# Optimization experiments

Hardware: AMD Instinct MI355X
Metric: run time of the kernel (lower is better)

## Reference

```python
import jax, jax.numpy as jnp
import numpy as np

N_NODES = 50000
N_EDGES = 800000
D_IN = 128
D_HID = 128
D_OUT = 1
N_GRAPHS = 64


def gcn_conv(x, edge_index, W, b):
    """PyG GCNConv: add self-loops, symmetric deg^-1/2 normalization, xW, scatter-add, +bias."""
    n = x.shape[0]
    loops = jnp.arange(n, dtype=edge_index.dtype)
    row = jnp.concatenate([edge_index[0], loops])  # source nodes
    col = jnp.concatenate([edge_index[1], loops])  # destination nodes
    deg = jax.ops.segment_sum(jnp.ones_like(col, dtype=x.dtype), col, num_segments=n)
    dinv = jax.lax.rsqrt(jnp.maximum(deg, 1.0))  # deg >= 1 due to self-loops
    norm = dinv[row] * dinv[col]                 # [E+N]
    h = x @ W                                    # [N, d_out] dense GEMM first (cheaper than per-edge)
    msgs = h[row] * norm[:, None]                # gather + scale, [E+N, d_out]
    out = jax.ops.segment_sum(msgs, col, num_segments=n)  # scatter-add
    return out + b


def setup_inputs() -> dict:
    key = jax.random.key(0)
    ks = jax.random.split(key, 12)
    x = jax.random.normal(ks[0], (N_NODES, D_IN), dtype=jnp.float32)
    edge_index = jax.random.randint(ks[1], (2, N_EDGES), 0, N_NODES, dtype=jnp.int64)
    batch = jnp.sort(jax.random.randint(ks[2], (N_NODES,), 0, N_GRAPHS, dtype=jnp.int64))
    s_in = 1.0 / np.sqrt(D_IN)
    s_hid = 1.0 / np.sqrt(D_HID)
    W0 = jax.random.uniform(ks[3], (D_IN, D_HID), jnp.float32, -s_in, s_in)
    b0 = jnp.zeros((D_HID,), jnp.float32)
    W1 = jax.random.uniform(ks[4], (D_HID, D_HID), jnp.float32, -s_hid, s_hid)
    b1 = jnp.zeros((D_HID,), jnp.float32)
    W2 = jax.random.uniform(ks[5], (D_HID, D_HID), jnp.float32, -s_hid, s_hid)
    b2 = jnp.zeros((D_HID,), jnp.float32)
    fc_w = jax.random.uniform(ks[6], (D_HID, D_OUT), jnp.float32, -s_hid, s_hid)
    fc_b = jax.random.uniform(ks[7], (D_OUT,), jnp.float32, -s_hid, s_hid)
    return {"x": x, "edge_index": edge_index, "batch": batch,
            "W0": W0, "b0": b0, "W1": W1, "b1": b1, "W2": W2, "b2": b2,
            "fc_w": fc_w, "fc_b": fc_b}


def reference(x, edge_index, batch, W0, b0, W1, b1, W2, b2, fc_w, fc_b):
    h = x
    for W, b in ((W0, b0), (W1, b1), (W2, b2)):  # 3 GCN layers (structural, not data loop)
        h = jax.nn.relu(gcn_conv(h, edge_index, W, b))
    # global_mean_pool over graph ids
    sums = jax.ops.segment_sum(h, batch, num_segments=N_GRAPHS)          # [G, d]
    counts = jax.ops.segment_sum(jnp.ones((h.shape[0],), h.dtype), batch, num_segments=N_GRAPHS)
    pooled = sums / jnp.maximum(counts, 1.0)[:, None]
    return pooled @ fc_w + fc_b  # [G, 1]
```

## Files before the change

### kernel.cpp

```cpp
#include <hip/hip_runtime.h>

#define DH 128
#define NGRAPH 64
#define NSHARD 8

static __device__ __forceinline__ float4 f4fma(float a, float4 b, float4 c) {
  c.x = fmaf(a, b.x, c.x); c.y = fmaf(a, b.y, c.y);
  c.z = fmaf(a, b.z, c.z); c.w = fmaf(a, b.w, c.w);
  return c;
}

__global__ void count_k(const int* __restrict__ col, int* __restrict__ deg8,
                        const int* __restrict__ batch, int* __restrict__ gcnt,
                        int e, int n) {
  int i = blockIdx.x * blockDim.x + threadIdx.x;
  if (i < e) {
    atomicAdd(&deg8[(blockIdx.x & (NSHARD - 1)) * n + col[i]], 1);
  }
  bool active = (i < n);
  int g = active ? batch[i] : 0;
  unsigned long long act = __ballot(active);
  if (!active) return;
  int first = __ffsll((long long)act) - 1;
  int g0 = __shfl(g, first);
  bool uni = __all(g == g0);
  int lane = threadIdx.x & 63;
  if (uni) {
    if (lane == first) atomicAdd(&gcnt[g], (int)__popcll(act));
  } else {
    atomicAdd(&gcnt[g], 1);
  }
}

__global__ __launch_bounds__(512) void scan1_k(const int* __restrict__ deg8, int* __restrict__ deg_tot,
                                               int* __restrict__ incl, int* __restrict__ blksum, int n) {
  __shared__ int s[512];
  int t = threadIdx.x;
  int i = blockIdx.x * 512 + t;
  int v = 0;
  if (i < n) {
    #pragma unroll
    for (int c = 0; c < NSHARD; ++c) v += deg8[c * n + i];
    deg_tot[i] = v;
  }
  s[t] = v;
  __syncthreads();
  #pragma unroll
  for (int off = 1; off < 512; off <<= 1) {
    int x = (t >= off) ? s[t - off] : 0;
    __syncthreads();
    s[t] += x;
    __syncthreads();
  }
  if (i < n) incl[i] = s[t];
  if (t == 511) blksum[blockIdx.x] = s[511];
}

__global__ __launch_bounds__(128) void scan2_k(int* __restrict__ blksum, int nb) {
  __shared__ int s[128];
  int t = threadIdx.x;
  int v = (t < nb) ? blksum[t] : 0;
  s[t] = v;
  __syncthreads();
  #pragma unroll
  for (int off = 1; off < 128; off <<= 1) {
    int x = (t >= off) ? s[t - off] : 0;
    __syncthreads();
    s[t] += x;
    __syncthreads();
  }
  if (t < nb) blksum[t] = s[t] - v;
}

__global__ __launch_bounds__(512) void scan3_k(const int* __restrict__ deg_tot, int* __restrict__ csr_ptr,
                                               const int* __restrict__ blkoff, int* __restrict__ cursor,
                                               float* __restrict__ dinv, int n, int e) {
  int i = blockIdx.x * 512 + threadIdx.x;
  if (i < n) {
    int cnt = deg_tot[i];
    int excl = csr_ptr[i] - cnt + blkoff[i >> 9];
    csr_ptr[i] = excl;
    cursor[i] = excl;
    dinv[i] = rsqrtf((float)(cnt + 1));
  }
  if (i == 0) csr_ptr[n] = e;
}

__global__ void scatter_k(const int* __restrict__ row, const int* __restrict__ col,
                          int* __restrict__ cursor, int* __restrict__ csr_src, int e) {
  int i = blockIdx.x * blockDim.x + threadIdx.x;
  if (i < e) {
    int c = col[i];
    int pos = atomicAdd(&cursor[c], 1);
    csr_src[pos] = row[i];
  }
}

__global__ __launch_bounds__(256) void gemm_k(const float* __restrict__ A, const float* __restrict__ W,
                                              const float* __restrict__ dinv,
                                              float* __restrict__ C, int M) {
  __shared__ float ws4[32][128];
  const int tid = threadIdx.x;
  const int tx = tid & 31;
  const int ty = tid >> 5;
  const int m_base = blockIdx.x * 64;

  const float* ar[8];
  #pragma unroll
  for (int i = 0; i < 8; i++) {
    int r = m_base + ty * 8 + i;
    if (r >= M) r = M - 1;
    ar[i] = A + (size_t)r * DH;
  }

  float4 acc[8];
  #pragma unroll
  for (int i = 0; i < 8; i++) acc[i] = make_float4(0.f, 0.f, 0.f, 0.f);

  for (int kc = 0; kc < 128; kc += 32) {
    const float4* Wg = (const float4*)(W + kc * DH);
    float4* wsv = (float4*)ws4;
    wsv[tid] = Wg[tid];
    wsv[tid + 256] = Wg[tid + 256];
    wsv[tid + 512] = Wg[tid + 512];
    wsv[tid + 768] = Wg[tid + 768];
    __syncthreads();
    #pragma unroll
    for (int k = 0; k < 32; k += 4) {
      float4 wb0 = *(const float4*)&ws4[k + 0][tx * 4];
      float4 wb1 = *(const float4*)&ws4[k + 1][tx * 4];
      float4 wb2 = *(const float4*)&ws4[k + 2][tx * 4];
      float4 wb3 = *(const float4*)&ws4[k + 3][tx * 4];
      #pragma unroll
      for (int i = 0; i < 8; i++) {
        float4 xa = *(const float4*)(ar[i] + kc + k);
        acc[i] = f4fma(xa.x, wb0, acc[i]);
        acc[i] = f4fma(xa.y, wb1, acc[i]);
        acc[i] = f4fma(xa.z, wb2, acc[i]);
        acc[i] = f4fma(xa.w, wb3, acc[i]);
      }
    }
    __syncthreads();
  }
  #pragma unroll
  for (int i = 0; i < 8; i++) {
    int r = m_base + ty * 8 + i;
    int rc = (r < M) ? r : (M - 1);
    float dsc = dinv[rc];
    acc[i].x *= dsc; acc[i].y *= dsc; acc[i].z *= dsc; acc[i].w *= dsc;
    *(float4*)(C + (size_t)r * DH + tx * 4) = acc[i];
  }
}

__global__ __launch_bounds__(256) void aggregate_k(const float* __restrict__ hs, const float* __restrict__ dinv,
                                                   const int* __restrict__ ptr, const int* __restrict__ csr_src,
                                                   const float* __restrict__ bias, float* __restrict__ out, int n) {
  int wave = threadIdx.x >> 6;
  int lane = threadIdx.x & 63;
  int node = blockIdx.x * 4 + wave;
  if (node >= n) return;
  const float2* h2 = (const float2*)hs;
  float di = dinv[node];
  int e0 = ptr[node], e1 = ptr[node + 1];
  float2 a0 = h2[(size_t)node * 64 + lane];
  float2 a1 = make_float2(0.f, 0.f), a2 = a1, a3 = a1, a4 = a1, a5 = a1, a6 = a1, a7 = a1;
  int e = e0;
  for (; e + 8 <= e1; e += 8) {
    int s0 = csr_src[e + 0], s1 = csr_src[e + 1], s2 = csr_src[e + 2], s3 = csr_src[e + 3];
    int s4 = csr_src[e + 4], s5 = csr_src[e + 5], s6 = csr_src[e + 6], s7 = csr_src[e + 7];
    float2 v0 = h2[(size_t)s0 * 64 + lane];
    float2 v1 = h2[(size_t)s1 * 64 + lane];
    float2 v2 = h2[(size_t)s2 * 64 + lane];
    float2 v3 = h2[(size_t)s3 * 64 + lane];
    float2 v4 = h2[(size_t)s4 * 64 + lane];
    float2 v5 = h2[(size_t)s5 * 64 + lane];
    float2 v6 = h2[(size_t)s6 * 64 + lane];
    float2 v7 = h2[(size_t)s7 * 64 + lane];
    a0.x += v0.x; a0.y += v0.y;
    a1.x += v1.x; a1.y += v1.y;
    a2.x += v2.x; a2.y += v2.y;
    a3.x += v3.x; a3.y += v3.y;
    a4.x += v4.x; a4.y += v4.y;
    a5.x += v5.x; a5.y += v5.y;
    a6.x += v6.x; a6.y += v6.y;
    a7.x += v7.x; a7.y += v7.y;
  }
  for (; e + 4 <= e1; e += 4) {
    int s0 = csr_src[e + 0], s1 = csr_src[e + 1], s2 = csr_src[e + 2], s3 = csr_src[e + 3];
    float2 v0 = h2[(size_t)s0 * 64 + lane];
    float2 v1 = h2[(size_t)s1 * 64 + lane];
    float2 v2 = h2[(size_t)s2 * 64 + lane];
    float2 v3 = h2[(size_t)s3 * 64 + lane];
    a0.x += v0.x; a0.y += v0.y;
    a1.x += v1.x; a1.y += v1.y;
    a2.x += v2.x; a2.y += v2.y;
    a3.x += v3.x; a3.y += v3.y;
  }
  for (; e < e1; ++e) {
    int s = csr_src[e];
    float2 v = h2[(size_t)s * 64 + lane];
    a0.x += v.x; a0.y += v.y;
  }
  float sx = ((a0.x + a1.x) + (a2.x + a3.x)) + ((a4.x + a5.x) + (a6.x + a7.x));
  float sy = ((a0.y + a1.y) + (a2.y + a3.y)) + ((a4.y + a5.y) + (a6.y + a7.y));
  float2 b = *(const float2*)(bias + lane * 2);
  sx = fmaxf(fmaf(sx, di, b.x), 0.f);
  sy = fmaxf(fmaf(sy, di, b.y), 0.f);
  ((float2*)out)[(size_t)node * 64 + lane] = make_float2(sx, sy);
}

#define POOL_CHUNK 50
__global__ __launch_bounds__(128) void pool_partial_k(const float* __restrict__ h, const int* __restrict__ batch,
                                                      float* __restrict__ pooled, int n) {
  int n0 = blockIdx.x * POOL_CHUNK;
  if (n0 >= n) return;
  int n1 = n0 + POOL_CHUNK; if (n1 > n) n1 = n;
  int d = threadIdx.x;
  float acc = 0.f;
  int gp = batch[n0];
  for (int i = n0; i < n1; ++i) {
    int g = batch[i];
    if (g != gp) { atomicAdd(&pooled[(size_t)gp * DH + d], acc); acc = 0.f; gp = g; }
    acc += h[(size_t)i * DH + d];
  }
  atomicAdd(&pooled[(size_t)gp * DH + d], acc);
}

__global__ void final_k(const float* __restrict__ pooled, const int* __restrict__ gcnt,
                        const float* __restrict__ fcw, const float* __restrict__ fcb,
                        float* __restrict__ out) {
  int g = threadIdx.x;
  if (g >= NGRAPH) return;
  float c = fmaxf((float)gcnt[g], 1.f);
  float s = 0.f;
  #pragma unroll 4
  for (int d = 0; d < DH; ++d) s = fmaf(pooled[(size_t)g * DH + d] / c, fcw[d], s);
  out[g] = s + fcb[0];
}

extern "C" void kernel_launch(void* const* d_in, const int* in_sizes, int n_in,
                              void* d_out, int out_size, void* d_ws, size_t ws_size,
                              hipStream_t stream) {
  const float* x    = (const float*)d_in[0];
  const int*   ei   = (const int*)d_in[1];
  const int*   batch= (const int*)d_in[2];
  const float* W0   = (const float*)d_in[3];
  const float* b0   = (const float*)d_in[4];
  const float* W1   = (const float*)d_in[5];
  const float* b1   = (const float*)d_in[6];
  const float* W2   = (const float*)d_in[7];
  const float* b2   = (const float*)d_in[8];
  const float* fcw  = (const float*)d_in[9];
  const float* fcb  = (const float*)d_in[10];
  float* out = (float*)d_out;

  const int N = in_sizes[0] / DH;
  const int E = in_sizes[1] / 2;
  const int* row = ei;
  const int* col = ei + E;
  const int MPAD = ((N + 63) / 64) * 64;

  char* ws = (char*)d_ws;
  size_t off = 0;
  auto carve = [&](size_t bytes) -> char* {
    char* p = ws + off;
    off = (off + bytes + 255) & ~(size_t)255;
    return p;
  };
  float* bufA    = (float*)carve((size_t)MPAD * DH * 4);
  float* bufB    = (float*)carve((size_t)MPAD * DH * 4);
  int*   deg8    = (int*)carve((size_t)NSHARD * N * 4);
  int*   deg_tot = (int*)carve((size_t)N * 4);
  float* dinv    = (float*)carve((size_t)N * 4);
  int*   csr_ptr = (int*)carve((size_t)(N + 1) * 4);
  int*   cursor  = (int*)carve((size_t)N * 4);
  int*   csr_src = (int*)carve((size_t)E * 4);
  int*   blksum  = (int*)carve(128 * 4);
  int*   gcnt    = (int*)carve(NGRAPH * 4);
  float* pooled  = (float*)carve((size_t)NGRAPH * DH * 4);
  (void)ws_size; (void)n_in; (void)out_size;

  const int nb256E = (E + 255) / 256;
  const int nbScan = (N + 511) / 512;

  hipMemsetAsync(deg8, 0, (size_t)NSHARD * N * 4, stream);
  hipMemsetAsync(gcnt, 0, NGRAPH * 4 + (size_t)NGRAPH * DH * 4, stream);

  count_k<<<nb256E, 256, 0, stream>>>(col, deg8, batch, gcnt, E, N);
  scan1_k<<<nbScan, 512, 0, stream>>>(deg8, deg_tot, csr_ptr, blksum, N);
  scan2_k<<<1, 128, 0, stream>>>(blksum, nbScan);
  scan3_k<<<nbScan, 512, 0, stream>>>(deg_tot, csr_ptr, blksum, cursor, dinv, N, E);
  scatter_k<<<nb256E, 256, 0, stream>>>(row, col, cursor, csr_src, E);

  const int gemmBlocks = MPAD / 64;
  const int aggBlocks = (N + 3) / 4;

  gemm_k<<<gemmBlocks, 256, 0, stream>>>(x, W0, dinv, bufA, N);
  aggregate_k<<<aggBlocks, 256, 0, stream>>>(bufA, dinv, csr_ptr, csr_src, b0, bufB, N);
  gemm_k<<<gemmBlocks, 256, 0, stream>>>(bufB, W1, dinv, bufA, N);
  aggregate_k<<<aggBlocks, 256, 0, stream>>>(bufA, dinv, csr_ptr, csr_src, b1, bufB, N);
  gemm_k<<<gemmBlocks, 256, 0, stream>>>(bufB, W2, dinv, bufA, N);
  aggregate_k<<<aggBlocks, 256, 0, stream>>>(bufA, dinv, csr_ptr, csr_src, b2, bufB, N);

  const int poolBlocks = (N + POOL_CHUNK - 1) / POOL_CHUNK;
  pool_partial_k<<<poolBlocks, 128, 0, stream>>>(bufB, batch, pooled, N);
  final_k<<<1, 64, 0, stream>>>(pooled, gcnt, fcw, fcb, out);
}
```

Before: 503.3 us.

## Overlap first GEMM with degree counting and shard scatter cursors

```diff
diff --git a/kernel.cpp b/kernel.cpp
--- a/kernel.cpp
+++ b/kernel.cpp
@@ -10,100 +10,15 @@
   return c;
 }
 
-__global__ void count_k(const int* __restrict__ col, int* __restrict__ deg8,
-                        const int* __restrict__ batch, int* __restrict__ gcnt,
-                        int e, int n) {
-  int i = blockIdx.x * blockDim.x + threadIdx.x;
-  if (i < e) {
-    atomicAdd(&deg8[(blockIdx.x & (NSHARD - 1)) * n + col[i]], 1);
-  }
-  bool active = (i < n);
-  int g = active ? batch[i] : 0;
-  unsigned long long act = __ballot(active);
-  if (!active) return;
-  int first = __ffsll((long long)act) - 1;
-  int g0 = __shfl(g, first);
-  bool uni = __all(g == g0);
-  int lane = threadIdx.x & 63;
-  if (uni) {
-    if (lane == first) atomicAdd(&gcnt[g], (int)__popcll(act));
-  } else {
-    atomicAdd(&gcnt[g], 1);
-  }
-}
-
-__global__ __launch_bounds__(512) void scan1_k(const int* __restrict__ deg8, int* __restrict__ deg_tot,
-                                               int* __restrict__ incl, int* __restrict__ blksum, int n) {
-  __shared__ int s[512];
-  int t = threadIdx.x;
-  int i = blockIdx.x * 512 + t;
-  int v = 0;
-  if (i < n) {
-    #pragma unroll
-    for (int c = 0; c < NSHARD; ++c) v += deg8[c * n + i];
-    deg_tot[i] = v;
-  }
-  s[t] = v;
-  __syncthreads();
-  #pragma unroll
-  for (int off = 1; off < 512; off <<= 1) {
-    int x = (t >= off) ? s[t - off] : 0;
-    __syncthreads();
-    s[t] += x;
-    __syncthreads();
-  }
-  if (i < n) incl[i] = s[t];
-  if (t == 511) blksum[blockIdx.x] = s[511];
-}
-
-__global__ __launch_bounds__(128) void scan2_k(int* __restrict__ blksum, int nb) {
-  __shared__ int s[128];
-  int t = threadIdx.x;
-  int v = (t < nb) ? blksum[t] : 0;
-  s[t] = v;
-  __syncthreads();
-  #pragma unroll
-  for (int off = 1; off < 128; off <<= 1) {
-    int x = (t >= off) ? s[t - off] : 0;
-    __syncthreads();
-    s[t] += x;
-    __syncthreads();
-  }
-  if (t < nb) blksum[t] = s[t] - v;
-}
-
-__global__ __launch_bounds__(512) void scan3_k(const int* __restrict__ deg_tot, int* __restrict__ csr_ptr,
-                                               const int* __restrict__ blkoff, int* __restrict__ cursor,
-                                               float* __restrict__ dinv, int n, int e) {
-  int i = blockIdx.x * 512 + threadIdx.x;
-  if (i < n) {
-    int cnt = deg_tot[i];
-    int excl = csr_ptr[i] - cnt + blkoff[i >> 9];
-    csr_ptr[i] = excl;
-    cursor[i] = excl;
-    dinv[i] = rsqrtf((float)(cnt + 1));
-  }
-  if (i == 0) csr_ptr[n] = e;
-}
-
-__global__ void scatter_k(const int* __restrict__ row, const int* __restrict__ col,
-                          int* __restrict__ cursor, int* __restrict__ csr_src, int e) {
-  int i = blockIdx.x * blockDim.x + threadIdx.x;
-  if (i < e) {
-    int c = col[i];
-    int pos = atomicAdd(&cursor[c], 1);
-    csr_src[pos] = row[i];
-  }
-}
-
-__global__ __launch_bounds__(256) void gemm_k(const float* __restrict__ A, const float* __restrict__ W,
-                                              const float* __restrict__ dinv,
-                                              float* __restrict__ C, int M) {
+template<bool SCALE>
+static __device__ __forceinline__ void gemm_body(const float* __restrict__ A, const float* __restrict__ W,
+                                                 const float* __restrict__ dinv, float* __restrict__ C,
+                                                 int M, int blk) {
   __shared__ float ws4[32][128];
   const int tid = threadIdx.x;
   const int tx = tid & 31;
   const int ty = tid >> 5;
-  const int m_base = blockIdx.x * 64;
+  const int m_base = blk * 64;
 
   const float* ar[8];
   #pragma unroll
@@ -145,11 +60,133 @@
   #pragma unroll
   for (int i = 0; i < 8; i++) {
     int r = m_base + ty * 8 + i;
-    int rc = (r < M) ? r : (M - 1);
-    float dsc = dinv[rc];
-    acc[i].x *= dsc; acc[i].y *= dsc; acc[i].z *= dsc; acc[i].w *= dsc;
+    if (SCALE) {
+      int rc = (r < M) ? r : (M - 1);
+      float dsc = dinv[rc];
+      acc[i].x *= dsc; acc[i].y *= dsc; acc[i].z *= dsc; acc[i].w *= dsc;
+    }
     *(float4*)(C + (size_t)r * DH + tx * 4) = acc[i];
   }
+}
+
+__global__ __launch_bounds__(256) void mega1_k(const float* __restrict__ x, const float* __restrict__ W0,
+                                               float* __restrict__ bufA, int M, int gemmBlocks,
+                                               const int* __restrict__ col, int* __restrict__ deg8,
+                                               const int* __restrict__ batch, int* __restrict__ gcnt,
+                                               int e, int n) {
+  if ((int)blockIdx.x < gemmBlocks) {
+    gemm_body<false>(x, W0, nullptr, bufA, M, blockIdx.x);
+    return;
+  }
+  int bi = blockIdx.x - gemmBlocks;
+  int i = bi * 256 + threadIdx.x;
+  if (i < e) {
+    atomicAdd(&deg8[(bi & (NSHARD - 1)) * n + col[i]], 1);
+  }
+  bool active = (i < n);
+  int g = active ? batch[i] : 0;
+  unsigned long long act = __ballot(active);
+  if (!active) return;
+  int first = __ffsll((long long)act) - 1;
+  int g0 = __shfl(g, first);
+  bool uni = __all(g == g0);
+  int lane = threadIdx.x & 63;
+  if (uni) {
+    if (lane == first) atomicAdd(&gcnt[g], (int)__popcll(act));
+  } else {
+    atomicAdd(&gcnt[g], 1);
+  }
+}
+
+__global__ __launch_bounds__(512) void scan1_k(const int* __restrict__ deg8, int* __restrict__ cur8,
+                                               int* __restrict__ deg_tot, int* __restrict__ incl,
+                                               int* __restrict__ blksum, int n) {
+  __shared__ int s[512];
+  int t = threadIdx.x;
+  int i = blockIdx.x * 512 + t;
+  int run = 0;
+  if (i < n) {
+    #pragma unroll
+    for (int c = 0; c < NSHARD; ++c) {
+      int d = deg8[c * n + i];
+      cur8[c * n + i] = run;
+      run += d;
+    }
+    deg_tot[i] = run;
+  }
+  s[t] = run;
+  __syncthreads();
+  #pragma unroll
+  for (int off = 1; off < 512; off <<= 1) {
+    int x = (t >= off) ? s[t - off] : 0;
+    __syncthreads();
+    s[t] += x;
+    __syncthreads();
+  }
+  if (i < n) incl[i] = s[t];
+  if (t == 511) blksum[blockIdx.x] = s[511];
+}
+
+__global__ __launch_bounds__(128) void scan2_k(int* __restrict__ blksum, int nb) {
+  __shared__ int s[128];
+  int t = threadIdx.x;
+  int v = (t < nb) ? blksum[t] : 0;
+  s[t] = v;
+  __syncthreads();
+  #pragma unroll
+  for (int off = 1; off < 128; off <<= 1) {
+    int x = (t >= off) ? s[t - off] : 0;
+    __syncthreads();
+    s[t] += x;
+    __syncthreads();
+  }
+  if (t < nb) blksum[t] = s[t] - v;
+}
+
+__global__ __launch_bounds__(512) void scan3_k(const int* __restrict__ deg_tot, int* __restrict__ csr_ptr,
+                                               const int* __restrict__ blkoff, int* __restrict__ cur8,
+                                               float* __restrict__ dinv, int n, int e) {
+  int i = blockIdx.x * 512 + threadIdx.x;
+  if (i < n) {
+    int cnt = deg_tot[i];
+    int excl = csr_ptr[i] - cnt + blkoff[i >> 9];
+    csr_ptr[i] = excl;
+    #pragma unroll
+    for (int c = 0; c < NSHARD; ++c) cur8[c * n + i] += excl;
+    dinv[i] = rsqrtf((float)(cnt + 1));
+  }
+  if (i == 0) csr_ptr[n] = e;
+}
+
+__global__ __launch_bounds__(256) void mega2_k(const int* __restrict__ row, const int* __restrict__ col,
+                                               int* __restrict__ cur8, int* __restrict__ csr_src,
+                                               int e, int n, int scatBlocks,
+                                               float* __restrict__ bufA, const float* __restrict__ dinv,
+                                               int nvec4) {
+  if ((int)blockIdx.x < scatBlocks) {
+    int bi = blockIdx.x;
+    int i = bi * 256 + threadIdx.x;
+    if (i < e) {
+      int c = col[i];
+      int pos = atomicAdd(&cur8[(bi & (NSHARD - 1)) * n + c], 1);
+      csr_src[pos] = row[i];
+    }
+    return;
+  }
+  int idx = (blockIdx.x - scatBlocks) * 256 + threadIdx.x;
+  if (idx < nvec4) {
+    int r = idx >> 5;
+    float4 v = ((const float4*)bufA)[idx];
+    float d = dinv[r];
+    v.x *= d; v.y *= d; v.z *= d; v.w *= d;
+    ((float4*)bufA)[idx] = v;
+  }
+}
+
+__global__ __launch_bounds__(256) void gemm_scaled_k(const float* __restrict__ A, const float* __restrict__ W,
+                                                     const float* __restrict__ dinv,
+                                                     float* __restrict__ C, int M) {
+  gemm_body<true>(A, W, dinv, C, M, blockIdx.x);
 }
 
 __global__ __launch_bounds__(256) void aggregate_k(const float* __restrict__ hs, const float* __restrict__ dinv,
@@ -270,36 +307,37 @@
   float* bufA    = (float*)carve((size_t)MPAD * DH * 4);
   float* bufB    = (float*)carve((size_t)MPAD * DH * 4);
   int*   deg8    = (int*)carve((size_t)NSHARD * N * 4);
+  int*   cur8    = (int*)carve((size_t)NSHARD * N * 4);
   int*   deg_tot = (int*)carve((size_t)N * 4);
   float* dinv    = (float*)carve((size_t)N * 4);
   int*   csr_ptr = (int*)carve((size_t)(N + 1) * 4);
-  int*   cursor  = (int*)carve((size_t)N * 4);
   int*   csr_src = (int*)carve((size_t)E * 4);
   int*   blksum  = (int*)carve(128 * 4);
   int*   gcnt    = (int*)carve(NGRAPH * 4);
   float* pooled  = (float*)carve((size_t)NGRAPH * DH * 4);
   (void)ws_size; (void)n_in; (void)out_size;
 
-  const int nb256E = (E + 255) / 256;
+  const int CB = (E + 255) / 256;
   const int nbScan = (N + 511) / 512;
+  const int gemmBlocks = MPAD / 64;
+  const int aggBlocks = (N + 3) / 4;
+  const int NV4 = N * 32;
+  const int SCB = (NV4 + 255) / 256;
 
   hipMemsetAsync(deg8, 0, (size_t)NSHARD * N * 4, stream);
   hipMemsetAsync(gcnt, 0, NGRAPH * 4 + (size_t)NGRAPH * DH * 4, stream);
 
-  count_k<<<nb256E, 256, 0, stream>>>(col, deg8, batch, gcnt, E, N);
-  scan1_k<<<nbScan, 512, 0, stream>>>(deg8, deg_tot, csr_ptr, blksum, N);
+  mega1_k<<<gemmBlocks + CB, 256, 0, stream>>>(x, W0, bufA, N, gemmBlocks,
+                                               col, deg8, batch, gcnt, E, N);
+  scan1_k<<<nbScan, 512, 0, stream>>>(deg8, cur8, deg_tot, csr_ptr, blksum, N);
   scan2_k<<<1, 128, 0, stream>>>(blksum, nbScan);
-  scan3_k<<<nbScan, 512, 0, stream>>>(deg_tot, csr_ptr, blksum, cursor, dinv, N, E);
-  scatter_k<<<nb256E, 256, 0, stream>>>(row, col, cursor, csr_src, E);
-
-  const int gemmBlocks = MPAD / 64;
-  const int aggBlocks = (N + 3) / 4;
-
-  gemm_k<<<gemmBlocks, 256, 0, stream>>>(x, W0, dinv, bufA, N);
+  scan3_k<<<nbScan, 512, 0, stream>>>(deg_tot, csr_ptr, blksum, cur8, dinv, N, E);
+  mega2_k<<<CB + SCB, 256, 0, stream>>>(row, col, cur8, csr_src, E, N, CB, bufA, dinv, NV4);
+
   aggregate_k<<<aggBlocks, 256, 0, stream>>>(bufA, dinv, csr_ptr, csr_src, b0, bufB, N);
-  gemm_k<<<gemmBlocks, 256, 0, stream>>>(bufB, W1, dinv, bufA, N);
+  gemm_scaled_k<<<gemmBlocks, 256, 0, stream>>>(bufB, W1, dinv, bufA, N);
   aggregate_k<<<aggBlocks, 256, 0, stream>>>(bufA, dinv, csr_ptr, csr_src, b1, bufB, N);
-  gemm_k<<<gemmBlocks, 256, 0, stream>>>(bufB, W2, dinv, bufA, N);
+  gemm_scaled_k<<<gemmBlocks, 256, 0, stream>>>(bufB, W2, dinv, bufA, N);
   aggregate_k<<<aggBlocks, 256, 0, stream>>>(bufA, dinv, csr_ptr, csr_src, b2, bufB, N);
 
   const int poolBlocks = (N + POOL_CHUNK - 1) / POOL_CHUNK;
```

Result: no change. 505.2 us (+0.4%).
